# Optimization experiments

Measured on AMD Instinct MI355X. Metric: run time of the kernel, lower is better.

The kernel has to match this reference:

```python
import jax, jax.numpy as jnp
import numpy as np

H = W = 56; WS = 7; SHIFT = 3; HEADS = 4; DIM = 128
HD = DIM // HEADS; SCALE = HD ** -0.5
NW = (H // WS) * (W // WS)  # 64 windows per image
N = WS * WS                 # 49 tokens per window
HID = int(DIM * 4.0)


def _rel_index():
    coords = np.stack(np.meshgrid(np.arange(WS), np.arange(WS), indexing='ij'))  # (2,WS,WS)
    cf = coords.reshape(2, -1)
    rel = (cf[:, :, None] - cf[:, None, :]).transpose(1, 2, 0)  # (N,N,2)
    rel[:, :, 0] += WS - 1
    rel[:, :, 1] += WS - 1
    rel[:, :, 0] *= 2 * WS - 1
    return jnp.asarray(rel.sum(-1))  # (N,N) int indices into bias table


def _attn_mask():
    img = np.zeros((H, W))
    cnt = 0
    for hs in (slice(0, -WS), slice(-WS, -SHIFT), slice(-SHIFT, None)):
        for ws in (slice(0, -WS), slice(-WS, -SHIFT), slice(-SHIFT, None)):
            img[hs, ws] = cnt
            cnt += 1
    mw = img.reshape(H // WS, WS, W // WS, WS).transpose(0, 2, 1, 3).reshape(-1, N)
    diff = mw[:, None, :] - mw[:, :, None]
    return jnp.asarray(np.where(diff != 0, -100.0, 0.0).astype(np.float32))  # (NW,N,N)

REL_IDX = _rel_index()
ATTN_MASK = _attn_mask()


def _ln(x, g, b):
    m = jnp.mean(x, -1, keepdims=True)
    v = jnp.var(x, -1, keepdims=True)
    return (x - m) * jax.lax.rsqrt(v + 1e-5) * g + b


def _win_part(x):  # (B,H,W,C) -> (B*NW, N, C)
    B = x.shape[0]
    x = x.reshape(B, H // WS, WS, W // WS, WS, DIM)
    return x.transpose(0, 1, 3, 2, 4, 5).reshape(-1, N, DIM)


def _win_rev(x, B):  # (B*NW, N, C) -> (B,H,W,C)
    x = x.reshape(B, H // WS, W // WS, WS, WS, DIM)
    return x.transpose(0, 1, 3, 2, 4, 5).reshape(B, H, W, DIM)


def setup_inputs() -> dict:
    key = jax.random.key(0)
    ks = jax.random.split(key, 8)
    s = 0.02
    return {
        'x': jax.random.normal(ks[0], (64, H * W, DIM), jnp.float32),
        'g1': jnp.ones((DIM,), jnp.float32),
        'b1': jnp.zeros((DIM,), jnp.float32),
        'qkv_w': jax.random.normal(ks[1], (3 * DIM, DIM), jnp.float32) * s,
        'qkv_b': jnp.zeros((3 * DIM,), jnp.float32),
        'rpb_table': jax.random.normal(ks[2], ((2 * WS - 1) ** 2, HEADS), jnp.float32) * s,
        'proj_w': jax.random.normal(ks[3], (DIM, DIM), jnp.float32) * s,
        'proj_b': jnp.zeros((DIM,), jnp.float32),
        'g2': jnp.ones((DIM,), jnp.float32),
        'b2': jnp.zeros((DIM,), jnp.float32),
        'fc1_w': jax.random.normal(ks[4], (HID, DIM), jnp.float32) * s,
        'fc1_b': jnp.zeros((HID,), jnp.float32),
        'fc2_w': jax.random.normal(ks[5], (DIM, HID), jnp.float32) * s,
        'fc2_b': jnp.zeros((DIM,), jnp.float32),
    }


def reference(x, g1, b1, qkv_w, qkv_b, rpb_table, proj_w, proj_b, g2, b2, fc1_w, fc1_b, fc2_w, fc2_b):
    B = x.shape[0]
    shortcut = x
    h = _ln(x, g1, b1).reshape(B, H, W, DIM)
    # cyclic shift + window partition
    h = jnp.roll(h, shift=(-SHIFT, -SHIFT), axis=(1, 2))
    xw = _win_part(h)  # (B*NW, N, C)
    B_ = xw.shape[0]
    # window attention
    qkv = (xw @ qkv_w.T + qkv_b).reshape(B_, N, 3, HEADS, HD).transpose(2, 0, 3, 1, 4)
    q, k, v = qkv[0] * SCALE, qkv[1], qkv[2]  # (B_, heads, N, hd)
    attn = jnp.einsum('bhnd,bhmd->bhnm', q, k)
    bias = rpb_table[REL_IDX.reshape(-1)].reshape(N, N, HEADS).transpose(2, 0, 1)  # (heads,N,N)
    attn = attn + bias[None]
    attn = attn.reshape(B, NW, HEADS, N, N) + ATTN_MASK[None, :, None]
    attn = jax.nn.softmax(attn.reshape(B_, HEADS, N, N), axis=-1)
    out = jnp.einsum('bhnm,bhmd->bhnd', attn, v).transpose(0, 2, 1, 3).reshape(B_, N, DIM)
    out = out @ proj_w.T + proj_b
    # reverse windows + reverse shift
    h = _win_rev(out, B)
    h = jnp.roll(h, shift=(SHIFT, SHIFT), axis=(1, 2)).reshape(B, H * W, DIM)
    x = shortcut + h
    # MLP
    y = _ln(x, g2, b2)
    y = jax.nn.gelu(y @ fc1_w.T + fc1_b, approximate=False)
    y = y @ fc2_w.T + fc2_b
    return x + y
```

## Files before the change

kernel.cpp:

```cpp
#include <hip/hip_runtime.h>

typedef unsigned int uint;
typedef unsigned short ushort;
using short8 = __attribute__((ext_vector_type(8))) short;
using f32x4  = __attribute__((ext_vector_type(4))) float;
using uint4v = __attribute__((ext_vector_type(4))) uint;

#define SCALE_ 0.17677669529663687f
#define MFMA(a,b,c) __builtin_amdgcn_mfma_f32_16x16x32_bf16(a,b,c,0,0,0)

__device__ inline ushort f2bf(float f){
  uint u = __float_as_uint(f);
  return (ushort)((u + 0x7fffu + ((u >> 16) & 1u)) >> 16);
}
__device__ inline uint pk2(float a, float b){
  return (uint)f2bf(a) | ((uint)f2bf(b) << 16);
}
__device__ inline float gelu(float v){
  return 0.5f * v * (1.f + erff(v * 0.70710678f));
}

__global__ __launch_bounds__(256) void prep_kernel(
    const float* __restrict__ qkv_w, const float* __restrict__ qkv_b,
    const float* __restrict__ rpb, const float* __restrict__ proj_w,
    const float* __restrict__ fc1_w, const float* __restrict__ fc2_w,
    ushort* __restrict__ qkv_wb, float* __restrict__ qkv_bs,
    ushort* __restrict__ proj_wb, ushort* __restrict__ fc1_wb,
    ushort* __restrict__ fc2_wb, float* __restrict__ T2)
{
  int i = blockIdx.x * 256 + threadIdx.x;
  if (i < 49152) qkv_wb[i] = f2bf(qkv_w[i] * (i < 16384 ? SCALE_ : 1.f));
  if (i < 16384) proj_wb[i] = f2bf(proj_w[i]);
  if (i < 65536) { fc1_wb[i] = f2bf(fc1_w[i]); fc2_wb[i] = f2bf(fc2_w[i]); }
  if (i < 384)   qkv_bs[i] = qkv_b[i] * (i < 128 ? SCALE_ : 1.f);
  if (i < 65536) {
    int cls = i >> 14, h = (i >> 12) & 3, tok = (i >> 6) & 63, key = i & 63;
    float val = -30000.f;
    if (tok < 49 && key < 49) {
      int ri = tok / 7, ci = tok - ri * 7, rj = key / 7, cj = key - rj * 7;
      val = rpb[((ri - rj + 6) * 13 + (ci - cj + 6)) * 4 + h];
      int er = cls >> 1, ec = cls & 1;
      int regi = (er ? (ri < 4 ? 1 : 2) : 0) * 3 + (ec ? (ci < 4 ? 1 : 2) : 0);
      int regj = (er ? (rj < 4 ? 1 : 2) : 0) * 3 + (ec ? (cj < 4 ? 1 : 2) : 0);
      if (regi != regj) val -= 100.f;
    }
    T2[i] = val;
  }
}

__global__ __launch_bounds__(256, 2) void attn_kernel(
    const float* __restrict__ x, const float* __restrict__ g1, const float* __restrict__ b1,
    const ushort* __restrict__ qkv_wb, const float* __restrict__ qkv_bs,
    const float* __restrict__ T2, const ushort* __restrict__ proj_wb,
    const float* __restrict__ proj_b, float* __restrict__ x_new)
{
  __shared__ __align__(16) char smem[25088];
  char*   xls = smem;
  ushort* oa  = (ushort*)smem;
  float*  Rp  = (float*)smem;
  const int tid = threadIdx.x;
  const int w = tid >> 6, lane = tid & 63;
  const int g = lane >> 4, li = lane & 15;
  const int blk = blockIdx.x;
  const int b = blk >> 6, wi = blk & 63;
  const int wr = wi >> 3, wc = wi & 7;
  const float* xb = x + (size_t)b * (3136 * 128);
  const f32x4 zf = {0.f, 0.f, 0.f, 0.f};
  const int srcA = ((g & 1) << 5) + li;
  const int srcB = srcA + 16;
  const int hi = g >> 1;

#pragma unroll
  for (int it = 0; it < 7; ++it) {
    int gi = it * 256 + tid;
    bool ok = gi < 1568;
    int t = ok ? (gi >> 5) : 48;
    int ch4 = (gi & 31) << 2;
    int tr = t / 7, tc = t - tr * 7;
    int rr = wr * 7 + tr + 3; rr -= (rr >= 56) ? 56 : 0;
    int cc = wc * 7 + tc + 3; cc -= (cc >= 56) ? 56 : 0;
    float4 v = *(const float4*)(xb + (size_t)(rr * 56 + cc) * 128 + ch4);
    float s = v.x + v.y + v.z + v.w;
    float s2 = v.x*v.x + v.y*v.y + v.z*v.z + v.w*v.w;
#pragma unroll
    for (int off = 16; off; off >>= 1) { s += __shfl_xor(s, off); s2 += __shfl_xor(s2, off); }
    float mn = s * 0.0078125f;
    float rs = rsqrtf(s2 * 0.0078125f - mn * mn + 1e-5f);
    if (ok) {
      float4 gg = *(const float4*)(g1 + ch4);
      float4 bb = *(const float4*)(b1 + ch4);
      uint2 u;
      u.x = pk2((v.x - mn) * rs * gg.x + bb.x, (v.y - mn) * rs * gg.y + bb.y);
      u.y = pk2((v.z - mn) * rs * gg.z + bb.z, (v.w - mn) * rs * gg.w + bb.w);
      int slot = ch4 >> 3;
      int tokx = t ^ ((slot & 7) << 1);
      *(uint2*)(xls + (slot * 64 + tokx) * 16 + ((ch4 & 4) << 1)) = u;
    }
  }
  if (tid < 240) {
    int slot = tid & 15, t = 49 + (tid >> 4);
    int tokx = t ^ ((slot & 7) << 1);
    uint4 z = make_uint4(0u, 0u, 0u, 0u);
    *(uint4*)(xls + (slot * 64 + tokx) * 16) = z;
  }
  __syncthreads();

  uint2 qp[2][4], kp[2][4];
  {
    f32x4 qacc[2][4], kacc[2][4];
#pragma unroll
    for (int cf = 0; cf < 2; ++cf)
#pragma unroll
      for (int m = 0; m < 4; ++m) { qacc[cf][m] = zf; kacc[cf][m] = zf; }
#pragma unroll
    for (int kt = 0; kt < 4; ++kt) {
      const int slot = kt * 4 + g;
      short8 xf[4];
#pragma unroll
      for (int m = 0; m < 4; ++m)
        xf[m] = *(const short8*)(xls + (slot * 64 + ((m * 16 + li) ^ ((slot & 7) << 1))) * 16);
      const int wofs = kt * 32 + g * 8;
#pragma unroll
      for (int cf = 0; cf < 2; ++cf) {
        short8 wq = *(const short8*)(qkv_wb + (size_t)(w * 32 + cf * 16 + li) * 128 + wofs);
#pragma unroll
        for (int m = 0; m < 4; ++m) qacc[cf][m] = MFMA(wq, xf[m], qacc[cf][m]);
      }
#pragma unroll
      for (int cf = 0; cf < 2; ++cf) {
        short8 wk = *(const short8*)(qkv_wb + (size_t)(128 + w * 32 + cf * 16 + li) * 128 + wofs);
#pragma unroll
        for (int m = 0; m < 4; ++m) kacc[cf][m] = MFMA(wk, xf[m], kacc[cf][m]);
      }
    }
#pragma unroll
    for (int cf = 0; cf < 2; ++cf) {
      f32x4 qb4 = *(const f32x4*)(qkv_bs + w * 32 + cf * 16 + g * 4);
      f32x4 kb4 = *(const f32x4*)(qkv_bs + 128 + w * 32 + cf * 16 + g * 4);
#pragma unroll
      for (int m = 0; m < 4; ++m) {
        f32x4 qv = qacc[cf][m] + qb4;
        qp[cf][m].x = pk2(qv[0], qv[1]); qp[cf][m].y = pk2(qv[2], qv[3]);
        f32x4 kv = kacc[cf][m] + kb4;
        kp[cf][m].x = pk2(kv[0], kv[1]); kp[cf][m].y = pk2(kv[2], kv[3]);
      }
    }
  }

  uint up[4][4][2];
  {
    const int cls = ((wr == 7) ? 2 : 0) | ((wc == 7) ? 1 : 0);
    const float* Tb = T2 + ((cls * 4 + w) << 12);
    short8 kf[4];
#pragma unroll
    for (int n = 0; n < 4; ++n) {
      uint a0 = __shfl(kp[0][n].x, srcA), a1 = __shfl(kp[0][n].y, srcA);
      uint a2 = __shfl(kp[0][n].x, srcB), a3 = __shfl(kp[0][n].y, srcB);
      uint b0 = __shfl(kp[1][n].x, srcA), b1 = __shfl(kp[1][n].y, srcA);
      uint b2 = __shfl(kp[1][n].x, srcB), b3 = __shfl(kp[1][n].y, srcB);
      uint4v u = { hi ? b0 : a0, hi ? b1 : a1, hi ? b2 : a2, hi ? b3 : a3 };
      kf[n] = __builtin_bit_cast(short8, u);
    }
#pragma unroll
    for (int m = 0; m < 4; ++m) {
      uint a0 = __shfl(qp[0][m].x, srcA), a1 = __shfl(qp[0][m].y, srcA);
      uint a2 = __shfl(qp[0][m].x, srcB), a3 = __shfl(qp[0][m].y, srcB);
      uint b0 = __shfl(qp[1][m].x, srcA), b1 = __shfl(qp[1][m].y, srcA);
      uint b2 = __shfl(qp[1][m].x, srcB), b3 = __shfl(qp[1][m].y, srcB);
      uint4v uq = { hi ? b0 : a0, hi ? b1 : a1, hi ? b2 : a2, hi ? b3 : a3 };
      short8 qf = __builtin_bit_cast(short8, uq);
      f32x4 s[4];
#pragma unroll
      for (int n = 0; n < 4; ++n) {
        s[n] = MFMA(kf[n], qf, zf);
        s[n] += *(const f32x4*)(Tb + (m * 16 + li) * 64 + n * 16 + g * 4);
      }
      float mx = -3.4e38f;
#pragma unroll
      for (int n = 0; n < 4; ++n)
        mx = fmaxf(mx, fmaxf(fmaxf(s[n][0], s[n][1]), fmaxf(s[n][2], s[n][3])));
      mx = fmaxf(mx, __shfl_xor(mx, 16));
      mx = fmaxf(mx, __shfl_xor(mx, 32));
      float sum = 0.f;
#pragma unroll
      for (int n = 0; n < 4; ++n)
#pragma unroll
        for (int r = 0; r < 4; ++r) { float e = __expf(s[n][r] - mx); s[n][r] = e; sum += e; }
      sum += __shfl_xor(sum, 16); sum += __shfl_xor(sum, 32);
      float rsm = 1.f / sum;
#pragma unroll
      for (int n = 0; n < 4; ++n) {
        up[m][n][0] = pk2(s[n][0] * rsm, s[n][1] * rsm);
        up[m][n][1] = pk2(s[n][2] * rsm, s[n][3] * rsm);
      }
    }
  }

  uint2 vp[4][2];
  {
    f32x4 vacc[4][2];
#pragma unroll
    for (int m = 0; m < 4; ++m) { vacc[m][0] = zf; vacc[m][1] = zf; }
#pragma unroll
    for (int kt = 0; kt < 4; ++kt) {
      const int slot = kt * 4 + g;
      short8 xf[4];
#pragma unroll
      for (int m = 0; m < 4; ++m)
        xf[m] = *(const short8*)(xls + (slot * 64 + ((m * 16 + li) ^ ((slot & 7) << 1))) * 16);
      const int wofs = kt * 32 + g * 8;
#pragma unroll
      for (int cf = 0; cf < 2; ++cf) {
        short8 wv = *(const short8*)(qkv_wb + (size_t)(256 + w * 32 + cf * 16 + li) * 128 + wofs);
#pragma unroll
        for (int m = 0; m < 4; ++m) vacc[m][cf] = MFMA(xf[m], wv, vacc[m][cf]);
      }
    }
#pragma unroll
    for (int cf = 0; cf < 2; ++cf) {
      float vb = qkv_bs[256 + w * 32 + cf * 16 + li];
#pragma unroll
      for (int m = 0; m < 4; ++m) {
        f32x4 vv = vacc[m][cf];
        vp[m][cf].x = pk2(vv[0] + vb, vv[1] + vb);
        vp[m][cf].y = pk2(vv[2] + vb, vv[3] + vb);
      }
    }
  }

  f32x4 oacc[2][4];
#pragma unroll
  for (int cf = 0; cf < 2; ++cf)
#pragma unroll
    for (int m = 0; m < 4; ++m) oacc[cf][m] = zf;
#pragma unroll
  for (int kt = 0; kt < 2; ++kt) {
    short8 vt[2];
#pragma unroll
    for (int half = 0; half < 2; ++half) {
      uint a0 = __shfl(vp[kt * 2][half].x, srcA), a1 = __shfl(vp[kt * 2][half].y, srcA);
      uint a2 = __shfl(vp[kt * 2][half].x, srcB), a3 = __shfl(vp[kt * 2][half].y, srcB);
      uint b0 = __shfl(vp[kt * 2 + 1][half].x, srcA), b1 = __shfl(vp[kt * 2 + 1][half].y, srcA);
      uint b2 = __shfl(vp[kt * 2 + 1][half].x, srcB), b3 = __shfl(vp[kt * 2 + 1][half].y, srcB);
      uint4v uv = { hi ? b0 : a0, hi ? b1 : a1, hi ? b2 : a2, hi ? b3 : a3 };
      vt[half] = __builtin_bit_cast(short8, uv);
    }
#pragma unroll
    for (int m = 0; m < 4; ++m) {
      uint t00 = __shfl(up[m][kt * 2][0], srcA),  t10 = __shfl(up[m][kt * 2 + 1][0], srcA);
      uint t01 = __shfl(up[m][kt * 2][1], srcA),  t11 = __shfl(up[m][kt * 2 + 1][1], srcA);
      uint t02 = __shfl(up[m][kt * 2][0], srcB),  t12 = __shfl(up[m][kt * 2 + 1][0], srcB);
      uint t03 = __shfl(up[m][kt * 2][1], srcB),  t13 = __shfl(up[m][kt * 2 + 1][1], srcB);
      uint4v pu = { hi ? t10 : t00, hi ? t11 : t01, hi ? t12 : t02, hi ? t13 : t03 };
      short8 pf = __builtin_bit_cast(short8, pu);
      oacc[0][m] = MFMA(vt[0], pf, oacc[0][m]);
      oacc[1][m] = MFMA(vt[1], pf, oacc[1][m]);
    }
  }
  __syncthreads();
#pragma unroll
  for (int cf = 0; cf < 2; ++cf)
#pragma unroll
    for (int m = 0; m < 4; ++m) {
      uint2 ou; ou.x = pk2(oacc[cf][m][0], oacc[cf][m][1]);
      ou.y = pk2(oacc[cf][m][2], oacc[cf][m][3]);
      *(uint2*)((char*)oa + ((m * 16 + li) * 136 + w * 32 + cf * 16 + g * 4) * 2) = ou;
    }
  __syncthreads();

  f32x4 pacc[2][4];
#pragma unroll
  for (int cf = 0; cf < 2; ++cf)
#pragma unroll
    for (int m = 0; m < 4; ++m) pacc[cf][m] = zf;
#pragma unroll
  for (int kt = 0; kt < 4; ++kt) {
    short8 af[4];
#pragma unroll
    for (int m = 0; m < 4; ++m)
      af[m] = *(const short8*)((char*)oa + (m * 16 + li) * 272 + kt * 64 + g * 16);
#pragma unroll
    for (int cf = 0; cf < 2; ++cf) {
      short8 wp = *(const short8*)(proj_wb + (size_t)(w * 32 + cf * 16 + li) * 128 + kt * 32 + g * 8);
#pragma unroll
      for (int m = 0; m < 4; ++m) pacc[cf][m] = MFMA(af[m], wp, pacc[cf][m]);
    }
  }
  __syncthreads();
#pragma unroll
  for (int cf = 0; cf < 2; ++cf) {
    int col = w * 32 + cf * 16 + li;
    float pb = proj_b[col];
#pragma unroll
    for (int m = 0; m < 4; ++m)
#pragma unroll
      for (int r = 0; r < 4; ++r) {
        int t2 = m * 16 + g * 4 + r;
        if (t2 < 49)
          Rp[t2 * 128 + (col ^ ((t2 & 7) << 2))] = pacc[cf][m][r] + pb;
      }
  }
  __syncthreads();

#pragma unroll
  for (int it = 0; it < 7; ++it) {
    int gi = it * 256 + tid;
    if (gi < 1568) {
      int t = gi >> 5, ch4 = (gi & 31) << 2;
      int tr = t / 7, tc = t - tr * 7;
      int rr = wr * 7 + tr + 3; rr -= (rr >= 56) ? 56 : 0;
      int cc = wc * 7 + tc + 3; cc -= (cc >= 56) ? 56 : 0;
      size_t off = ((size_t)b * 3136 + rr * 56 + cc) * 128 + ch4;
      f32x4 d = *(const f32x4*)&Rp[t * 128 + (ch4 ^ ((t & 7) << 2))];
      float4 xr = *(const float4*)(x + off);
      float4 ov;
      ov.x = xr.x + d[0]; ov.y = xr.y + d[1];
      ov.z = xr.z + d[2]; ov.w = xr.w + d[3];
      *(float4*)(x_new + off) = ov;
    }
  }
}

__global__ __launch_bounds__(256, 2) void mlp_kernel(
    float* __restrict__ xio,
    const float* __restrict__ g2, const float* __restrict__ b2,
    const ushort* __restrict__ w1, const float* __restrict__ fb1,
    const ushort* __restrict__ w2, const float* __restrict__ fb2)
{
  __shared__ __align__(16) char smem[32768];
  char* Axs = smem;
  char* hls = smem + 16384;
  float* Rp = (float*)smem;
  const int tid = threadIdx.x, lane = tid & 63, w = tid >> 6;
  const int g = lane >> 4, li = lane & 15;
  float* xw = xio + (size_t)blockIdx.x * 64 * 128;
  const f32x4 zf = {0.f, 0.f, 0.f, 0.f};

#pragma unroll
  for (int it = 0; it < 8; ++it) {
    int gi = it * 256 + tid;
    int row = gi >> 5, ch4 = (gi & 31) << 2;
    float4 v = *(const float4*)(xw + row * 128 + ch4);
    float s = v.x + v.y + v.z + v.w;
    float s2 = v.x*v.x + v.y*v.y + v.z*v.z + v.w*v.w;
#pragma unroll
    for (int off = 16; off; off >>= 1) { s += __shfl_xor(s, off); s2 += __shfl_xor(s2, off); }
    float mn = s * 0.0078125f;
    float rs = rsqrtf(s2 * 0.0078125f - mn * mn + 1e-5f);
    float4 gg = *(const float4*)(g2 + ch4);
    float4 bb = *(const float4*)(b2 + ch4);
    uint2 u;
    u.x = pk2((v.x - mn) * rs * gg.x + bb.x, (v.y - mn) * rs * gg.y + bb.y);
    u.y = pk2((v.z - mn) * rs * gg.z + bb.z, (v.w - mn) * rs * gg.w + bb.w);
    int slot = ch4 >> 3;
    int tokx = row ^ ((slot & 7) << 1);
    *(uint2*)(Axs + (slot * 64 + tokx) * 16 + ((ch4 & 4) << 1)) = u;
  }
  __syncthreads();

  f32x4 acc2[4][2];
#pragma unroll
  for (int mi = 0; mi < 4; ++mi) { acc2[mi][0] = zf; acc2[mi][1] = zf; }

  for (int ck = 0; ck < 4; ++ck) {
    f32x4 acc1[2][4];
#pragma unroll
    for (int oi = 0; oi < 2; ++oi)
#pragma unroll
      for (int mi = 0; mi < 4; ++mi) acc1[oi][mi] = zf;
#pragma unroll
    for (int kt = 0; kt < 4; ++kt) {
      const int slot = kt * 4 + g;
      short8 xf[4];
#pragma unroll
      for (int mi = 0; mi < 4; ++mi)
        xf[mi] = *(const short8*)(Axs + (slot * 64 + ((mi * 16 + li) ^ ((slot & 7) << 1))) * 16);
#pragma unroll
      for (int oi = 0; oi < 2; ++oi) {
        short8 wf = *(const short8*)(w1 + (size_t)(ck * 128 + w * 32 + oi * 16 + li) * 128 + kt * 32 + g * 8);
#pragma unroll
        for (int mi = 0; mi < 4; ++mi) acc1[oi][mi] = MFMA(wf, xf[mi], acc1[oi][mi]);
      }
    }
#pragma unroll
    for (int oi = 0; oi < 2; ++oi) {
      f32x4 b4 = *(const f32x4*)(fb1 + ck * 128 + w * 32 + oi * 16 + g * 4);
#pragma unroll
      for (int mi = 0; mi < 4; ++mi) {
        f32x4 h = acc1[oi][mi] + b4;
        uint2 u; u.x = pk2(gelu(h[0]), gelu(h[1])); u.y = pk2(gelu(h[2]), gelu(h[3]));
        *(uint2*)(hls + ((w * 4 + oi * 2 + (g >> 1)) * 64 + mi * 16 + li) * 16 + ((g & 1) << 3)) = u;
      }
    }
    __syncthreads();
#pragma unroll
    for (int kt = 0; kt < 4; ++kt) {
      short8 hf[4];
#pragma unroll
      for (int mi = 0; mi < 4; ++mi)
        hf[mi] = *(const short8*)(hls + ((kt * 4 + g) * 64 + mi * 16 + li) * 16);
#pragma unroll
      for (int bo = 0; bo < 2; ++bo) {
        short8 wf = *(const short8*)(w2 + (size_t)(w * 32 + bo * 16 + li) * 512 + ck * 128 + kt * 32 + g * 8);
#pragma unroll
        for (int mi = 0; mi < 4; ++mi) acc2[mi][bo] = MFMA(hf[mi], wf, acc2[mi][bo]);
      }
    }
    __syncthreads();
  }

#pragma unroll
  for (int mi = 0; mi < 4; ++mi)
#pragma unroll
    for (int bo = 0; bo < 2; ++bo) {
      int out = w * 32 + bo * 16 + li;
#pragma unroll
      for (int r = 0; r < 4; ++r) {
        int tok = mi * 16 + g * 4 + r;
        Rp[tok * 128 + (out ^ ((tok & 7) << 2))] = acc2[mi][bo][r];
      }
    }
  __syncthreads();
#pragma unroll
  for (int it = 0; it < 8; ++it) {
    int gi = it * 256 + tid;
    int row = gi >> 5, ch4 = (gi & 31) << 2;
    f32x4 d = *(const f32x4*)&Rp[row * 128 + (ch4 ^ ((row & 7) << 2))];
    float4 xr = *(const float4*)(xw + row * 128 + ch4);
    float4 bb = *(const float4*)(fb2 + ch4);
    float4 ov;
    ov.x = xr.x + d[0] + bb.x; ov.y = xr.y + d[1] + bb.y;
    ov.z = xr.z + d[2] + bb.z; ov.w = xr.w + d[3] + bb.w;
    *(float4*)(xw + row * 128 + ch4) = ov;
  }
}

extern "C" void kernel_launch(void* const* d_in, const int* in_sizes, int n_in,
                              void* d_out, int out_size, void* d_ws, size_t ws_size,
                              hipStream_t stream)
{
  const float* x      = (const float*)d_in[0];
  const float* g1     = (const float*)d_in[1];
  const float* b1     = (const float*)d_in[2];
  const float* qkv_w  = (const float*)d_in[3];
  const float* qkv_b  = (const float*)d_in[4];
  const float* rpb    = (const float*)d_in[5];
  const float* proj_w = (const float*)d_in[6];
  const float* proj_b = (const float*)d_in[7];
  const float* g2     = (const float*)d_in[8];
  const float* b2     = (const float*)d_in[9];
  const float* fc1_w  = (const float*)d_in[10];
  const float* fc1_b  = (const float*)d_in[11];
  const float* fc2_w  = (const float*)d_in[12];
  const float* fc2_b  = (const float*)d_in[13];

  char* ws = (char*)d_ws;
  float*  T2      = (float*)ws;
  ushort* qkv_wb  = (ushort*)(ws + 262144);
  ushort* proj_wb = (ushort*)(ws + 360448);
  ushort* fc1_wb  = (ushort*)(ws + 393216);
  ushort* fc2_wb  = (ushort*)(ws + 524288);
  float*  qkv_bs  = (float*)(ws + 655360);
  float* out = (float*)d_out;

  prep_kernel<<<256, 256, 0, stream>>>(qkv_w, qkv_b, rpb, proj_w, fc1_w, fc2_w,
                                       qkv_wb, qkv_bs, proj_wb, fc1_wb, fc2_wb, T2);
  attn_kernel<<<4096, 256, 0, stream>>>(x, g1, b1, qkv_wb, qkv_bs, T2,
                                        proj_wb, proj_b, out);
  mlp_kernel<<<3136, 256, 0, stream>>>(out, g2, b2, fc1_wb, fc1_b, fc2_wb, fc2_b);
}
```

Baseline: 318.6 us.

## Stream Q per row-tile through softmax and PV, store bias table in bf16

Reorders the attention kernel to compute K and V first and keep them in registers. Q is then computed one 16-token row tile at a time, fused with the scores, softmax and P·V accumulation. This avoids holding the full Q and probability matrices in registers at once, which cuts register pressure and live ranges. The combined bias/mask table is also stored in bf16 to halve its global traffic, at a small precision cost on bias values and some repeated weight loads for the Q projection.

```diff
diff --git a/kernel.cpp b/kernel.cpp
--- a/kernel.cpp
+++ b/kernel.cpp
@@ -26,7 +26,7 @@
     const float* __restrict__ fc1_w, const float* __restrict__ fc2_w,
     ushort* __restrict__ qkv_wb, float* __restrict__ qkv_bs,
     ushort* __restrict__ proj_wb, ushort* __restrict__ fc1_wb,
-    ushort* __restrict__ fc2_wb, float* __restrict__ T2)
+    ushort* __restrict__ fc2_wb, ushort* __restrict__ T2b)
 {
   int i = blockIdx.x * 256 + threadIdx.x;
   if (i < 49152) qkv_wb[i] = f2bf(qkv_w[i] * (i < 16384 ? SCALE_ : 1.f));
@@ -44,14 +44,14 @@
       int regj = (er ? (rj < 4 ? 1 : 2) : 0) * 3 + (ec ? (cj < 4 ? 1 : 2) : 0);
       if (regi != regj) val -= 100.f;
     }
-    T2[i] = val;
+    T2b[i] = f2bf(val);
   }
 }
 
 __global__ __launch_bounds__(256, 2) void attn_kernel(
     const float* __restrict__ x, const float* __restrict__ g1, const float* __restrict__ b1,
     const ushort* __restrict__ qkv_wb, const float* __restrict__ qkv_bs,
-    const float* __restrict__ T2, const ushort* __restrict__ proj_wb,
+    const ushort* __restrict__ T2b, const ushort* __restrict__ proj_wb,
     const float* __restrict__ proj_b, float* __restrict__ x_new)
 {
   __shared__ __align__(16) char smem[25088];
@@ -105,13 +105,13 @@
   }
   __syncthreads();
 
-  uint2 qp[2][4], kp[2][4];
+  short8 kf[4];
   {
-    f32x4 qacc[2][4], kacc[2][4];
+    f32x4 kacc[2][4];
 #pragma unroll
     for (int cf = 0; cf < 2; ++cf)
 #pragma unroll
-      for (int m = 0; m < 4; ++m) { qacc[cf][m] = zf; kacc[cf][m] = zf; }
+      for (int m = 0; m < 4; ++m) kacc[cf][m] = zf;
 #pragma unroll
     for (int kt = 0; kt < 4; ++kt) {
       const int slot = kt * 4 + g;
@@ -122,36 +122,21 @@
       const int wofs = kt * 32 + g * 8;
 #pragma unroll
       for (int cf = 0; cf < 2; ++cf) {
-        short8 wq = *(const short8*)(qkv_wb + (size_t)(w * 32 + cf * 16 + li) * 128 + wofs);
-#pragma unroll
-        for (int m = 0; m < 4; ++m) qacc[cf][m] = MFMA(wq, xf[m], qacc[cf][m]);
-      }
-#pragma unroll
-      for (int cf = 0; cf < 2; ++cf) {
         short8 wk = *(const short8*)(qkv_wb + (size_t)(128 + w * 32 + cf * 16 + li) * 128 + wofs);
 #pragma unroll
         for (int m = 0; m < 4; ++m) kacc[cf][m] = MFMA(wk, xf[m], kacc[cf][m]);
       }
     }
+    uint2 kp[2][4];
 #pragma unroll
     for (int cf = 0; cf < 2; ++cf) {
-      f32x4 qb4 = *(const f32x4*)(qkv_bs + w * 32 + cf * 16 + g * 4);
       f32x4 kb4 = *(const f32x4*)(qkv_bs + 128 + w * 32 + cf * 16 + g * 4);
 #pragma unroll
       for (int m = 0; m < 4; ++m) {
-        f32x4 qv = qacc[cf][m] + qb4;
-        qp[cf][m].x = pk2(qv[0], qv[1]); qp[cf][m].y = pk2(qv[2], qv[3]);
         f32x4 kv = kacc[cf][m] + kb4;
         kp[cf][m].x = pk2(kv[0], kv[1]); kp[cf][m].y = pk2(kv[2], kv[3]);
       }
     }
-  }
-
-  uint up[4][4][2];
-  {
-    const int cls = ((wr == 7) ? 2 : 0) | ((wc == 7) ? 1 : 0);
-    const float* Tb = T2 + ((cls * 4 + w) << 12);
-    short8 kf[4];
 #pragma unroll
     for (int n = 0; n < 4; ++n) {
       uint a0 = __shfl(kp[0][n].x, srcA), a1 = __shfl(kp[0][n].y, srcA);
@@ -161,19 +146,97 @@
       uint4v u = { hi ? b0 : a0, hi ? b1 : a1, hi ? b2 : a2, hi ? b3 : a3 };
       kf[n] = __builtin_bit_cast(short8, u);
     }
+  }
+
+  short8 vt[2][2];
+  {
+    f32x4 vacc[4][2];
+#pragma unroll
+    for (int m = 0; m < 4; ++m) { vacc[m][0] = zf; vacc[m][1] = zf; }
+#pragma unroll
+    for (int kt = 0; kt < 4; ++kt) {
+      const int slot = kt * 4 + g;
+      short8 xf[4];
+#pragma unroll
+      for (int m = 0; m < 4; ++m)
+        xf[m] = *(const short8*)(xls + (slot * 64 + ((m * 16 + li) ^ ((slot & 7) << 1))) * 16);
+      const int wofs = kt * 32 + g * 8;
+#pragma unroll
+      for (int cf = 0; cf < 2; ++cf) {
+        short8 wv = *(const short8*)(qkv_wb + (size_t)(256 + w * 32 + cf * 16 + li) * 128 + wofs);
+#pragma unroll
+        for (int m = 0; m < 4; ++m) vacc[m][cf] = MFMA(xf[m], wv, vacc[m][cf]);
+      }
+    }
+    uint2 vp[4][2];
+#pragma unroll
+    for (int cf = 0; cf < 2; ++cf) {
+      float vb = qkv_bs[256 + w * 32 + cf * 16 + li];
+#pragma unroll
+      for (int m = 0; m < 4; ++m) {
+        f32x4 vv = vacc[m][cf];
+        vp[m][cf].x = pk2(vv[0] + vb, vv[1] + vb);
+        vp[m][cf].y = pk2(vv[2] + vb, vv[3] + vb);
+      }
+    }
+#pragma unroll
+    for (int kt = 0; kt < 2; ++kt)
+#pragma unroll
+      for (int half = 0; half < 2; ++half) {
+        uint a0 = __shfl(vp[kt * 2][half].x, srcA), a1 = __shfl(vp[kt * 2][half].y, srcA);
+        uint a2 = __shfl(vp[kt * 2][half].x, srcB), a3 = __shfl(vp[kt * 2][half].y, srcB);
+        uint b0 = __shfl(vp[kt * 2 + 1][half].x, srcA), b1 = __shfl(vp[kt * 2 + 1][half].y, srcA);
+        uint b2 = __shfl(vp[kt * 2 + 1][half].x, srcB), b3 = __shfl(vp[kt * 2 + 1][half].y, srcB);
+        uint4v uv = { hi ? b0 : a0, hi ? b1 : a1, hi ? b2 : a2, hi ? b3 : a3 };
+        vt[kt][half] = __builtin_bit_cast(short8, uv);
+      }
+  }
+
+  f32x4 oacc[2][4];
+#pragma unroll
+  for (int cf = 0; cf < 2; ++cf)
+#pragma unroll
+    for (int m = 0; m < 4; ++m) oacc[cf][m] = zf;
+  {
+    const int cls = ((wr == 7) ? 2 : 0) | ((wc == 7) ? 1 : 0);
+    const ushort* Tb = T2b + ((cls * 4 + w) << 12);
+    const f32x4 qb40 = *(const f32x4*)(qkv_bs + w * 32 + g * 4);
+    const f32x4 qb41 = *(const f32x4*)(qkv_bs + w * 32 + 16 + g * 4);
 #pragma unroll
     for (int m = 0; m < 4; ++m) {
-      uint a0 = __shfl(qp[0][m].x, srcA), a1 = __shfl(qp[0][m].y, srcA);
-      uint a2 = __shfl(qp[0][m].x, srcB), a3 = __shfl(qp[0][m].y, srcB);
-      uint b0 = __shfl(qp[1][m].x, srcA), b1 = __shfl(qp[1][m].y, srcA);
-      uint b2 = __shfl(qp[1][m].x, srcB), b3 = __shfl(qp[1][m].y, srcB);
+      f32x4 qacc[2] = {zf, zf};
+#pragma unroll
+      for (int kt = 0; kt < 4; ++kt) {
+        const int slot = kt * 4 + g;
+        short8 xfm = *(const short8*)(xls + (slot * 64 + ((m * 16 + li) ^ ((slot & 7) << 1))) * 16);
+        const int wofs = kt * 32 + g * 8;
+        short8 wq0 = *(const short8*)(qkv_wb + (size_t)(w * 32 + li) * 128 + wofs);
+        short8 wq1 = *(const short8*)(qkv_wb + (size_t)(w * 32 + 16 + li) * 128 + wofs);
+        qacc[0] = MFMA(wq0, xfm, qacc[0]);
+        qacc[1] = MFMA(wq1, xfm, qacc[1]);
+      }
+      uint2 qpm[2];
+      {
+        f32x4 q0 = qacc[0] + qb40;
+        f32x4 q1 = qacc[1] + qb41;
+        qpm[0].x = pk2(q0[0], q0[1]); qpm[0].y = pk2(q0[2], q0[3]);
+        qpm[1].x = pk2(q1[0], q1[1]); qpm[1].y = pk2(q1[2], q1[3]);
+      }
+      uint a0 = __shfl(qpm[0].x, srcA), a1 = __shfl(qpm[0].y, srcA);
+      uint a2 = __shfl(qpm[0].x, srcB), a3 = __shfl(qpm[0].y, srcB);
+      uint b0 = __shfl(qpm[1].x, srcA), b1 = __shfl(qpm[1].y, srcA);
+      uint b2 = __shfl(qpm[1].x, srcB), b3 = __shfl(qpm[1].y, srcB);
       uint4v uq = { hi ? b0 : a0, hi ? b1 : a1, hi ? b2 : a2, hi ? b3 : a3 };
       short8 qf = __builtin_bit_cast(short8, uq);
       f32x4 s[4];
 #pragma unroll
       for (int n = 0; n < 4; ++n) {
         s[n] = MFMA(kf[n], qf, zf);
-        s[n] += *(const f32x4*)(Tb + (m * 16 + li) * 64 + n * 16 + g * 4);
+        uint2 tv = *(const uint2*)(Tb + (m * 16 + li) * 64 + n * 16 + g * 4);
+        s[n][0] += __uint_as_float(tv.x << 16);
+        s[n][1] += __uint_as_float(tv.x & 0xffff0000u);
+        s[n][2] += __uint_as_float(tv.y << 16);
+        s[n][3] += __uint_as_float(tv.y & 0xffff0000u);
       }
       float mx = -3.4e38f;
 #pragma unroll
@@ -188,73 +251,23 @@
         for (int r = 0; r < 4; ++r) { float e = __expf(s[n][r] - mx); s[n][r] = e; sum += e; }
       sum += __shfl_xor(sum, 16); sum += __shfl_xor(sum, 32);
       float rsm = 1.f / sum;
+      uint um[4][2];
 #pragma unroll
       for (int n = 0; n < 4; ++n) {
-        up[m][n][0] = pk2(s[n][0] * rsm, s[n][1] * rsm);
-        up[m][n][1] = pk2(s[n][2] * rsm, s[n][3] * rsm);
-      }
-    }
-  }
-
-  uint2 vp[4][2];
-  {
-    f32x4 vacc[4][2];
-#pragma unroll
-    for (int m = 0; m < 4; ++m) { vacc[m][0] = zf; vacc[m][1] = zf; }
-#pragma unroll
-    for (int kt = 0; kt < 4; ++kt) {
-      const int slot = kt * 4 + g;
-      short8 xf[4];
-#pragma unroll
-      for (int m = 0; m < 4; ++m)
-        xf[m] = *(const short8*)(xls + (slot * 64 + ((m * 16 + li) ^ ((slot & 7) << 1))) * 16);
-      const int wofs = kt * 32 + g * 8;
-#pragma unroll
-      for (int cf = 0; cf < 2; ++cf) {
-        short8 wv = *(const short8*)(qkv_wb + (size_t)(256 + w * 32 + cf * 16 + li) * 128 + wofs);
-#pragma unroll
-        for (int m = 0; m < 4; ++m) vacc[m][cf] = MFMA(xf[m], wv, vacc[m][cf]);
-      }
-    }
-#pragma unroll
-    for (int cf = 0; cf < 2; ++cf) {
-      float vb = qkv_bs[256 + w * 32 + cf * 16 + li];
-#pragma unroll
-      for (int m = 0; m < 4; ++m) {
-        f32x4 vv = vacc[m][cf];
-        vp[m][cf].x = pk2(vv[0] + vb, vv[1] + vb);
-        vp[m][cf].y = pk2(vv[2] + vb, vv[3] + vb);
-      }
-    }
-  }
-
-  f32x4 oacc[2][4];
-#pragma unroll
-  for (int cf = 0; cf < 2; ++cf)
-#pragma unroll
-    for (int m = 0; m < 4; ++m) oacc[cf][m] = zf;
-#pragma unroll
-  for (int kt = 0; kt < 2; ++kt) {
-    short8 vt[2];
-#pragma unroll
-    for (int half = 0; half < 2; ++half) {
-      uint a0 = __shfl(vp[kt * 2][half].x, srcA), a1 = __shfl(vp[kt * 2][half].y, srcA);
-      uint a2 = __shfl(vp[kt * 2][half].x, srcB), a3 = __shfl(vp[kt * 2][half].y, srcB);
-      uint b0 = __shfl(vp[kt * 2 + 1][half].x, srcA), b1 = __shfl(vp[kt * 2 + 1][half].y, srcA);
-      uint b2 = __shfl(vp[kt * 2 + 1][half].x, srcB), b3 = __shfl(vp[kt * 2 + 1][half].y, srcB);
-      uint4v uv = { hi ? b0 : a0, hi ? b1 : a1, hi ? b2 : a2, hi ? b3 : a3 };
-      vt[half] = __builtin_bit_cast(short8, uv);
-    }
-#pragma unroll
-    for (int m = 0; m < 4; ++m) {
-      uint t00 = __shfl(up[m][kt * 2][0], srcA),  t10 = __shfl(up[m][kt * 2 + 1][0], srcA);
-      uint t01 = __shfl(up[m][kt * 2][1], srcA),  t11 = __shfl(up[m][kt * 2 + 1][1], srcA);
-      uint t02 = __shfl(up[m][kt * 2][0], srcB),  t12 = __shfl(up[m][kt * 2 + 1][0], srcB);
-      uint t03 = __shfl(up[m][kt * 2][1], srcB),  t13 = __shfl(up[m][kt * 2 + 1][1], srcB);
-      uint4v pu = { hi ? t10 : t00, hi ? t11 : t01, hi ? t12 : t02, hi ? t13 : t03 };
-      short8 pf = __builtin_bit_cast(short8, pu);
-      oacc[0][m] = MFMA(vt[0], pf, oacc[0][m]);
-      oacc[1][m] = MFMA(vt[1], pf, oacc[1][m]);
+        um[n][0] = pk2(s[n][0] * rsm, s[n][1] * rsm);
+        um[n][1] = pk2(s[n][2] * rsm, s[n][3] * rsm);
+      }
+#pragma unroll
+      for (int kt = 0; kt < 2; ++kt) {
+        uint t00 = __shfl(um[kt * 2][0], srcA),  t10 = __shfl(um[kt * 2 + 1][0], srcA);
+        uint t01 = __shfl(um[kt * 2][1], srcA),  t11 = __shfl(um[kt * 2 + 1][1], srcA);
+        uint t02 = __shfl(um[kt * 2][0], srcB),  t12 = __shfl(um[kt * 2 + 1][0], srcB);
+        uint t03 = __shfl(um[kt * 2][1], srcB),  t13 = __shfl(um[kt * 2 + 1][1], srcB);
+        uint4v pu = { hi ? t10 : t00, hi ? t11 : t01, hi ? t12 : t02, hi ? t13 : t03 };
+        short8 pf = __builtin_bit_cast(short8, pu);
+        oacc[0][m] = MFMA(vt[kt][0], pf, oacc[0][m]);
+        oacc[1][m] = MFMA(vt[kt][1], pf, oacc[1][m]);
+      }
     }
   }
   __syncthreads();
@@ -455,7 +468,7 @@
   const float* fc2_b  = (const float*)d_in[13];
 
   char* ws = (char*)d_ws;
-  float*  T2      = (float*)ws;
+  ushort* T2b     = (ushort*)ws;
   ushort* qkv_wb  = (ushort*)(ws + 262144);
   ushort* proj_wb = (ushort*)(ws + 360448);
   ushort* fc1_wb  = (ushort*)(ws + 393216);
@@ -464,8 +477,8 @@
   float* out = (float*)d_out;
 
   prep_kernel<<<256, 256, 0, stream>>>(qkv_w, qkv_b, rpb, proj_w, fc1_w, fc2_w,
-                                       qkv_wb, qkv_bs, proj_wb, fc1_wb, fc2_wb, T2);
-  attn_kernel<<<4096, 256, 0, stream>>>(x, g1, b1, qkv_wb, qkv_bs, T2,
+                                       qkv_wb, qkv_bs, proj_wb, fc1_wb, fc2_wb, T2b);
+  attn_kernel<<<4096, 256, 0, stream>>>(x, g1, b1, qkv_wb, qkv_bs, T2b,
                                         proj_wb, proj_b, out);
   mlp_kernel<<<3136, 256, 0, stream>>>(out, g2, b2, fc1_wb, fc1_b, fc2_wb, fc2_b);
 }
```

After: 317.1 us. About the same (-0.5%).
